# Performance work log

Measured on AMD Instinct MI355X. Metric: run time of the kernel, lower is better.

Reference implementation:

```python
import jax, jax.numpy as jnp
import numpy as np


def _ste_round(r):
    # straight-through round
    return r + jax.lax.stop_gradient(jnp.round(r) - r)


def quant_sym(x, s, qn, qp):
    # symmetric LSQ-style fake-quant: clamp(round(x/s)) * s
    r = jnp.clip(x / s, qn, qp)
    return _ste_round(r) * s


def quant_asym(x, s, beta, qn, qp):
    # asymmetric fake-quant with learnable zero-point beta
    r = jnp.clip((x - beta) / s, qn, qp)
    return _ste_round(r) * s + beta


def quant_weight_statsq(w, n_bits=8):
    # statsq: per-output-channel scale from weight statistics
    qp = 2 ** (n_bits - 1) - 1          # 127
    qn = -(2 ** (n_bits - 1))           # -128
    s = 2.0 * jnp.mean(jnp.abs(w), axis=1, keepdims=True) / jnp.sqrt(float(qp))
    return quant_sym(w, s, qn, qp)


def setup_inputs() -> dict:
    key = jax.random.key(0)
    ks = jax.random.split(key, 8)
    B, N, C, H = 4, 4096, 1024, 4096
    x = jax.random.normal(ks[0], (B, N, C), dtype=jnp.float32)
    w1 = jax.random.normal(ks[1], (H, C), dtype=jnp.float32) * (1.0 / np.sqrt(C))
    b1 = jax.random.normal(ks[2], (H,), dtype=jnp.float32) * 0.01
    w2 = jax.random.normal(ks[3], (C, H), dtype=jnp.float32) * (1.0 / np.sqrt(H))
    b2 = jax.random.normal(ks[4], (C,), dtype=jnp.float32) * 0.01
    # learnable LSQ activation scales (per input channel), kept positive
    s_a1 = 0.05 + 0.05 * jax.random.uniform(ks[5], (C,), dtype=jnp.float32)
    s_a2 = 0.02 + 0.02 * jax.random.uniform(ks[6], (H,), dtype=jnp.float32)
    beta2 = jnp.zeros((H,), dtype=jnp.float32)
    return {"x": x, "w1": w1, "b1": b1, "w2": w2, "b2": b2,
            "s_a1": s_a1, "s_a2": s_a2, "beta2": beta2}


def reference(x, w1, b1, w2, b2, s_a1, s_a2, beta2):
    # fc1: symmetric 8-bit LSQ on input, statsq 8-bit on weight
    xq = quant_sym(x, s_a1, -128, 127)
    wq1 = quant_weight_statsq(w1)
    h = jnp.einsum('bnc,hc->bnh', xq, wq1) + b1
    h = jax.nn.gelu(h, approximate=False)  # nn.GELU default (exact erf)
    # drop1 = identity in eval
    # fc2: asymmetric 8-bit LSQ on (non-negative-skewed) activations
    hq = quant_asym(h, s_a2, beta2, 0, 255)
    wq2 = quant_weight_statsq(w2)
    out = jnp.einsum('bnh,ch->bnc', hq, wq2) + b2
    # drop2 = identity in eval
    return out
```

## Files before the change

kernel.cpp:

```cpp
#include <hip/hip_runtime.h>
#include <cstdint>
#include <cstddef>

typedef __attribute__((ext_vector_type(8))) short short8;
typedef __attribute__((ext_vector_type(4))) float f32x4;
typedef __attribute__((ext_vector_type(4))) unsigned short ushort4_t;

__device__ __forceinline__ unsigned short f2bf(float f) {
  unsigned u = __float_as_uint(f);
  u += 0x7FFFu + ((u >> 16) & 1u);
  return (unsigned short)(u >> 16);
}

__device__ __forceinline__ void gload_lds16(const void* g, void* lds) {
  __builtin_amdgcn_global_load_lds((const __attribute__((address_space(1))) void*)g,
                                   (__attribute__((address_space(3))) void*)lds,
                                   16, 0, 0);
}

__device__ __forceinline__ float erf_fast(float v) {
  float x = fabsf(v);
  float t = __builtin_amdgcn_rcpf(fmaf(0.3275911f, x, 1.0f));
  float p = fmaf(1.061405429f, t, -1.453152027f);
  p = fmaf(p, t, 1.421413741f);
  p = fmaf(p, t, -0.284496736f);
  p = fmaf(p, t, 0.254829592f);
  p = p * t;
  float e = fmaf(-p, __expf(-x * x), 1.0f);
  unsigned s = __float_as_uint(v) & 0x80000000u;
  return __uint_as_float(__float_as_uint(e) | s);
}

__global__ void quant_x_kernel(const float4* __restrict__ x, const float* __restrict__ s_a1,
                               ushort4_t* __restrict__ xq, int n4, int c4mask) {
  const int stride = gridDim.x * blockDim.x;
  for (int i = blockIdx.x * blockDim.x + threadIdx.x; i < n4; i += stride) {
    float4 v = x[i];
    int c = (i & c4mask) << 2;
    float vv[4] = {v.x, v.y, v.z, v.w};
    ushort4_t o;
#pragma unroll
    for (int j = 0; j < 4; ++j) {
      float s = s_a1[c + j];
      float r = vv[j] / s;
      r = fminf(fmaxf(r, -128.f), 127.f);
      o[j] = f2bf(rintf(r) * s);
    }
    xq[i] = o;
  }
}

__global__ void quant_w_kernel(const float* __restrict__ w, unsigned short* __restrict__ wq,
                               int cols) {
  const int row = blockIdx.x;
  const float* wr = w + (size_t)row * cols;
  float part = 0.f;
  for (int j = threadIdx.x; j < cols; j += blockDim.x) part += fabsf(wr[j]);
#pragma unroll
  for (int o = 32; o > 0; o >>= 1) part += __shfl_down(part, o, 64);
  __shared__ float wsum[4];
  if ((threadIdx.x & 63) == 0) wsum[threadIdx.x >> 6] = part;
  __syncthreads();
  float mean = (wsum[0] + wsum[1] + wsum[2] + wsum[3]) / (float)cols;
  float s = 2.f * mean / sqrtf(127.f);
  unsigned short* wqr = wq + (size_t)row * cols;
  for (int j = threadIdx.x; j < cols; j += blockDim.x) {
    float r = wr[j] / s;
    r = fminf(fmaxf(r, -128.f), 127.f);
    wqr[j] = f2bf(rintf(r) * s);
  }
}

#define BAR() __builtin_amdgcn_s_barrier()
#define SB() __builtin_amdgcn_sched_barrier(0)
#define LGKM0() { asm volatile("s_waitcnt lgkmcnt(0)" ::: "memory"); SB(); }
#define PRIO1() __builtin_amdgcn_s_setprio(1)
#define PRIO0() __builtin_amdgcn_s_setprio(0)

#define STG(gbase, ldsbuf, h, kt) { \
  _Pragma("unroll") for (int i_ = 0; i_ < 2; ++i_) { \
    const int rb_ = (h) * 128 + (w * 2 + i_) * 8; \
    gload_lds16((gbase) + (size_t)rb_ * K + (size_t)(kt) * 64, (void*)((ldsbuf) + rb_ * 64)); } }

#define LDA_(dst, buf, mh) { \
  _Pragma("unroll") for (int mi_ = 0; mi_ < 4; ++mi_) { \
    dst[mi_][0] = *(const short8*)((buf) + aBase + (mh) * 4096 + mi_ * 1024 + ck0); \
    dst[mi_][1] = *(const short8*)((buf) + aBase + (mh) * 4096 + mi_ * 1024 + ck1); } }

#define LDBX(dst, buf, base) { \
  _Pragma("unroll") for (int ni_ = 0; ni_ < 2; ++ni_) { \
    dst[ni_][0] = *(const short8*)((buf) + (base) + ni_ * 1024 + ck0); \
    dst[ni_][1] = *(const short8*)((buf) + (base) + ni_ * 1024 + ck1); } }

#define MMQ(aR, bR, mh, nh) { \
  _Pragma("unroll") for (int kk_ = 0; kk_ < 2; ++kk_) \
  _Pragma("unroll") for (int mi_ = 0; mi_ < 4; ++mi_) \
  _Pragma("unroll") for (int ni_ = 0; ni_ < 2; ++ni_) \
    acc[(mh) * 4 + mi_][(nh) * 2 + ni_] = __builtin_amdgcn_mfma_f32_16x16x32_bf16( \
        aR[mi_][kk_], bR[ni_][kk_], acc[(mh) * 4 + mi_][(nh) * 2 + ni_], 0, 0, 0); }

template <int EPI>
__global__ __launch_bounds__(512, 2) void gemm_bt_m2(
    const unsigned short* __restrict__ A, const unsigned short* __restrict__ B,
    const float* __restrict__ bias, const float* __restrict__ s2,
    const float* __restrict__ beta, unsigned short* __restrict__ Cq,
    float* __restrict__ Cf, int N, int K)
{
  __shared__ __align__(16) unsigned short As0[256 * 64];
  __shared__ __align__(16) unsigned short As1[256 * 64];
  __shared__ __align__(16) unsigned short Bs0[256 * 64];
  __shared__ __align__(16) unsigned short Bs1[256 * 64];

  const int tid = threadIdx.x;
  const int w = tid >> 6, ll = tid & 63;
  const int wr = w >> 2, wc = w & 3;

  const int nwg = gridDim.x * gridDim.y;
  const int bid = blockIdx.x + gridDim.x * blockIdx.y;
  const int cpx = nwg >> 3;
  const int swz = (bid & 7) * cpx + (bid >> 3);
  const int gy = gridDim.y;
  const int bx = swz / gy, by = swz - bx * gy;
  const long bm = (long)bx * 256;
  const long bn = (long)by * 256;

  const int srow = ll >> 3;
  const int scol = ((ll & 7) ^ srow) << 3;
  const unsigned short* Agl = A + ((size_t)bm + srow) * K + scol;
  const unsigned short* Bgl = B + ((size_t)bn + srow) * K + scol;

  const int lhi = ll >> 4, llo = ll & 15, l7 = ll & 7;
  const int ck0 = ((0 * 4 + lhi) ^ l7) * 8;
  const int ck1 = ((1 * 4 + lhi) ^ l7) * 8;
  const int aBase = (wr * 128 + llo) * 64;
  const int bBase0 = (wc * 32 + llo) * 64;
  const int bBase1 = (128 + wc * 32 + llo) * 64;

  f32x4 acc[8][4] = {};
  short8 a0[4][2], a1[4][2], b0[2][2], b1[2][2];

  const int nkt = K >> 6;

  STG(Bgl, Bs0, 0, 0); STG(Agl, As0, 0, 0); STG(Agl, As0, 1, 0); STG(Bgl, Bs0, 1, 0);
  STG(Bgl, Bs1, 0, 1); STG(Agl, As1, 0, 1); STG(Agl, As1, 1, 1); STG(Bgl, Bs1, 1, 1);
  asm volatile("s_waitcnt vmcnt(8)" ::: "memory"); SB();
  BAR();
  LDBX(b0, Bs0, bBase0);
  LGKM0();
  BAR();

  for (int t = 0; t < nkt; ++t) {
    unsigned short* Asb = (t & 1) ? As1 : As0;
    unsigned short* Bsb = (t & 1) ? Bs1 : Bs0;
    unsigned short* Bsn = (t & 1) ? Bs0 : Bs1;
    const bool i1 = (t + 1 < nkt), i2 = (t + 2 < nkt);

    LDA_(a0, Asb, 0);
    if (i2) STG(Bgl, Bsb, 0, t + 2);
    BAR(); LGKM0();
    PRIO1(); MMQ(a0, b0, 0, 0); PRIO0();
    BAR();

    LDA_(a1, Asb, 1);
    if (i2) STG(Agl, Asb, 0, t + 2);
    BAR(); LGKM0();
    PRIO1(); MMQ(a1, b0, 1, 0); PRIO0();
    BAR();

    LDBX(b1, Bsb, bBase1);
    if (i2) STG(Agl, Asb, 1, t + 2);
    BAR(); LGKM0();
    PRIO1(); MMQ(a1, b1, 1, 1); PRIO0();
    BAR();

    if (i1) LDBX(b0, Bsn, bBase0);
    if (i2) STG(Bgl, Bsb, 1, t + 2);
    if (i2)      { asm volatile("s_waitcnt vmcnt(6)" ::: "memory"); SB(); }
    else if (i1) { asm volatile("s_waitcnt vmcnt(0)" ::: "memory"); SB(); }
    BAR(); LGKM0();
    PRIO1(); MMQ(a0, b1, 0, 1); PRIO0();
    BAR();
  }

  const int lr = lhi;
  const int lc = llo;
#pragma unroll
  for (int NI = 0; NI < 4; ++NI) {
    const long col = bn + wc * 32 + ((NI >= 2) ? 128 : 0) + (NI & 1) * 16 + lc;
    const float bv = bias[col];
    float sv = 1.f, bev = 0.f, inv = 1.f;
    if (EPI == 0) { sv = s2[col]; bev = beta[col]; inv = 1.0f / sv; }
#pragma unroll
    for (int MI = 0; MI < 8; ++MI) {
#pragma unroll
      for (int r = 0; r < 4; ++r) {
        const size_t rowg = (size_t)(bm + wr * 128 + MI * 16 + lr * 4 + r);
        float v = acc[MI][NI][r] + bv;
        if (EPI == 0) {
          float g = 0.5f * v * (1.f + erf_fast(v * 0.70710678118654752f));
          float rr = (g - bev) * inv;
          rr = fminf(fmaxf(rr, 0.f), 255.f);
          Cq[rowg * N + col] = f2bf(fmaf(rintf(rr), sv, bev));
        } else {
          Cf[rowg * N + col] = v;
        }
      }
    }
  }
}

extern "C" void kernel_launch(void* const* d_in, const int* in_sizes, int n_in,
                              void* d_out, int out_size, void* d_ws, size_t ws_size,
                              hipStream_t stream) {
  const float* x     = (const float*)d_in[0];
  const float* w1    = (const float*)d_in[1];
  const float* b1    = (const float*)d_in[2];
  const float* w2    = (const float*)d_in[3];
  const float* b2    = (const float*)d_in[4];
  const float* s_a1  = (const float*)d_in[5];
  const float* s_a2  = (const float*)d_in[6];
  const float* beta2 = (const float*)d_in[7];
  float* out = (float*)d_out;

  const int C = 1024, H = 4096;
  const int M = in_sizes[0] / C;

  unsigned short* xq  = (unsigned short*)d_ws;
  unsigned short* wq1 = xq  + (size_t)M * C;
  unsigned short* wq2 = wq1 + (size_t)H * C;
  unsigned short* hq  = wq2 + (size_t)C * H;

  quant_x_kernel<<<2048, 256, 0, stream>>>((const float4*)x, s_a1, (ushort4_t*)xq,
                                           M * C / 4, C / 4 - 1);
  quant_w_kernel<<<H, 256, 0, stream>>>(w1, wq1, C);
  quant_w_kernel<<<C, 256, 0, stream>>>(w2, wq2, H);

  dim3 g1(M / 256, H / 256);
  gemm_bt_m2<0><<<g1, 512, 0, stream>>>(xq, wq1, b1, s_a2, beta2, hq, nullptr, H, C);
  dim3 g2(M / 256, C / 256);
  gemm_bt_m2<1><<<g2, 512, 0, stream>>>(hq, wq2, b2, nullptr, nullptr, nullptr, out, C, H);
}
```

Measured before the change: 370.4 us.

## Restructure GEMM main loop to overlap LDS reads with MFMA phases

```diff
diff --git a/kernel.cpp b/kernel.cpp
--- a/kernel.cpp
+++ b/kernel.cpp
@@ -71,9 +71,10 @@
   }
 }
 
-#define BAR() __builtin_amdgcn_s_barrier()
+#define BAR() { asm volatile("" ::: "memory"); __builtin_amdgcn_s_barrier(); asm volatile("" ::: "memory"); }
 #define SB() __builtin_amdgcn_sched_barrier(0)
-#define LGKM0() { asm volatile("s_waitcnt lgkmcnt(0)" ::: "memory"); SB(); }
+#define LGKM(n) { asm volatile("s_waitcnt lgkmcnt(" #n ")" ::: "memory"); SB(); }
+#define VMC(n) { asm volatile("s_waitcnt vmcnt(" #n ")" ::: "memory"); SB(); }
 #define PRIO1() __builtin_amdgcn_s_setprio(1)
 #define PRIO0() __builtin_amdgcn_s_setprio(0)
 
@@ -100,7 +101,7 @@
         aR[mi_][kk_], bR[ni_][kk_], acc[(mh) * 4 + mi_][(nh) * 2 + ni_], 0, 0, 0); }
 
 template <int EPI>
-__global__ __launch_bounds__(512, 2) void gemm_bt_m2(
+__global__ __launch_bounds__(512, 2) void gemm_bt_cf(
     const unsigned short* __restrict__ A, const unsigned short* __restrict__ B,
     const float* __restrict__ bias, const float* __restrict__ s2,
     const float* __restrict__ beta, unsigned short* __restrict__ Cq,
@@ -142,44 +143,42 @@
   const int nkt = K >> 6;
 
   STG(Bgl, Bs0, 0, 0); STG(Agl, As0, 0, 0); STG(Agl, As0, 1, 0); STG(Bgl, Bs0, 1, 0);
-  STG(Bgl, Bs1, 0, 1); STG(Agl, As1, 0, 1); STG(Agl, As1, 1, 1); STG(Bgl, Bs1, 1, 1);
-  asm volatile("s_waitcnt vmcnt(8)" ::: "memory"); SB();
+  STG(Bgl, Bs1, 0, 1); STG(Agl, As1, 0, 1); STG(Agl, As1, 1, 1);
+  VMC(6);
   BAR();
-  LDBX(b0, Bs0, bBase0);
-  LGKM0();
-  BAR();
+  LDA_(a0, As0, 0); SB();
+  LDBX(b1, Bs0, bBase1); SB();
 
   for (int t = 0; t < nkt; ++t) {
     unsigned short* Asb = (t & 1) ? As1 : As0;
     unsigned short* Bsb = (t & 1) ? Bs1 : Bs0;
+    unsigned short* Asn = (t & 1) ? As0 : As1;
     unsigned short* Bsn = (t & 1) ? Bs0 : Bs1;
     const bool i1 = (t + 1 < nkt), i2 = (t + 2 < nkt);
 
-    LDA_(a0, Asb, 0);
+    BAR();
+    LDBX(b0, Bsb, bBase0); SB();
+    if (i1) STG(Bgl, Bsn, 1, t + 1);
+    LGKM(0);
+    PRIO1(); MMQ(a0, b0, 0, 0); PRIO0();
+
+    BAR();
+    LDA_(a1, Asb, 1); SB();
     if (i2) STG(Bgl, Bsb, 0, t + 2);
-    BAR(); LGKM0();
-    PRIO1(); MMQ(a0, b0, 0, 0); PRIO0();
-    BAR();
-
-    LDA_(a1, Asb, 1);
+    PRIO1(); MMQ(a0, b1, 0, 1); PRIO0();
+
+    if (i2) { VMC(6); } else { VMC(0); }
+    BAR();
+    if (i1) { LDA_(a0, Asn, 0); SB(); }
     if (i2) STG(Agl, Asb, 0, t + 2);
-    BAR(); LGKM0();
+    if (i1) { LGKM(8); } else { LGKM(0); }
+    PRIO1(); MMQ(a1, b1, 1, 1); PRIO0();
+
+    if (i2) { VMC(4); } else { VMC(0); }
+    BAR();
+    if (i1) { LDBX(b1, Bsn, bBase1); SB(); }
+    if (i2) STG(Agl, Asb, 1, t + 2);
     PRIO1(); MMQ(a1, b0, 1, 0); PRIO0();
-    BAR();
-
-    LDBX(b1, Bsb, bBase1);
-    if (i2) STG(Agl, Asb, 1, t + 2);
-    BAR(); LGKM0();
-    PRIO1(); MMQ(a1, b1, 1, 1); PRIO0();
-    BAR();
-
-    if (i1) LDBX(b0, Bsn, bBase0);
-    if (i2) STG(Bgl, Bsb, 1, t + 2);
-    if (i2)      { asm volatile("s_waitcnt vmcnt(6)" ::: "memory"); SB(); }
-    else if (i1) { asm volatile("s_waitcnt vmcnt(0)" ::: "memory"); SB(); }
-    BAR(); LGKM0();
-    PRIO1(); MMQ(a0, b1, 0, 1); PRIO0();
-    BAR();
   }
 
   const int lr = lhi;
@@ -236,7 +235,7 @@
   quant_w_kernel<<<C, 256, 0, stream>>>(w2, wq2, H);
 
   dim3 g1(M / 256, H / 256);
-  gemm_bt_m2<0><<<g1, 512, 0, stream>>>(xq, wq1, b1, s_a2, beta2, hq, nullptr, H, C);
+  gemm_bt_cf<0><<<g1, 512, 0, stream>>>(xq, wq1, b1, s_a2, beta2, hq, nullptr, H, C);
   dim3 g2(M / 256, C / 256);
-  gemm_bt_m2<1><<<g2, 512, 0, stream>>>(hq, wq2, b2, nullptr, nullptr, nullptr, out, C, H);
-}
+  gemm_bt_cf<1><<<g2, 512, 0, stream>>>(hq, wq2, b2, nullptr, nullptr, nullptr, out, C, H);
+}
```

Measured after the change: 363.9 us. Within noise of the previous version (-1.8%).
